# Performance work log

Measured on AMD Instinct MI355X. Metric: run time of the kernel, lower is better.

## Reference

```python
import jax, jax.numpy as jnp
import numpy as np

NUM_GROUPS = 4
EPS = 1e-6


def group_norm(x, scale, bias):
    # x: (b, c, f, h, w), normalize per group over (c//G, f, h, w) in fp32
    b, c, f, h, w = x.shape
    xg = x.astype(jnp.float32).reshape(b, NUM_GROUPS, c // NUM_GROUPS, f, h, w)
    mean = xg.mean(axis=(2, 3, 4, 5), keepdims=True)
    var = xg.var(axis=(2, 3, 4, 5), keepdims=True)
    xn = ((xg - mean) * jax.lax.rsqrt(var + EPS)).reshape(b, c, f, h, w)
    return (xn * scale[None, :, None, None, None] + bias[None, :, None, None, None]).astype(x.dtype)


def conv1x1x1(x, w, b):
    # 1x1x1 Conv3d == channel-mixing linear. w: (c_out, c_in), b: (c_out,)
    return jnp.einsum('bcfhw,oc->bofhw', x, w) + b[None, :, None, None, None]


def setup_inputs() -> dict:
    key = jax.random.key(0)
    ks = jax.random.split(key, 9)
    c = 256
    x = jax.random.normal(ks[0], (6, c, 48, 48), dtype=jnp.float32)  # (3*b, c, h, w), b=2
    init = lambda k: (jax.random.normal(k, (c, c), dtype=jnp.float32) * 0.02)
    return {
        'x': x,
        'gn_scale': jnp.ones((c,), jnp.float32),
        'gn_bias': jnp.zeros((c,), jnp.float32),
        'wq': init(ks[1]), 'bq': jnp.zeros((c,), jnp.float32),
        'wk': init(ks[2]), 'bk': jnp.zeros((c,), jnp.float32),
        'wv': init(ks[3]), 'bv': jnp.zeros((c,), jnp.float32),
        'wp': init(ks[4]), 'bp': jnp.zeros((c,), jnp.float32),
    }


def reference(x, gn_scale, gn_bias, wq, bq, wk, bk, wv, bv, wp, bp):
    b3, c, hh, ww = x.shape
    b = b3 // 3
    # chunk(x, 3) along batch, stack at dim 2 -> (b, c, f=3, h, w)
    h_ = x.reshape(3, b, c, hh, ww).transpose(1, 2, 0, 3, 4)
    h_ = group_norm(h_, gn_scale, gn_bias)
    q = conv1x1x1(h_, wq, bq)
    k = conv1x1x1(h_, wk, bk)
    v = conv1x1x1(h_, wv, bv)
    f = 3
    n = f * hh * ww
    qf = q.reshape(b, c, n).transpose(0, 2, 1)  # (b, n, c)
    kf = k.reshape(b, c, n)                     # (b, c, n)
    vf = v.reshape(b, c, n)                     # (b, c, n)
    scale = jnp.float32(c) ** -0.5
    scores = jnp.einsum('bic,bcj->bij', qf.astype(jnp.float32), kf.astype(jnp.float32)) * scale
    attn = jax.nn.softmax(scores, axis=2).astype(x.dtype)  # (b, n, n)
    # bmm(v, attn^T): out[b,c,i] = sum_j v[b,c,j] * attn[b,i,j]
    h_ = jnp.einsum('bcj,bij->bci', vf, attn).reshape(b, c, f, hh, ww)
    h_ = conv1x1x1(h_, wp, bp)
    # (b, c, f, h, w) -> (b, f, c, h, w) -> (b*f, c, h, w)
    h_ = h_.transpose(0, 2, 1, 3, 4).reshape(b * f, c, hh, ww)
    return x + h_
```

## Files before the change

kernel.cpp:

```cpp
#include <hip/hip_runtime.h>
#include <hip/hip_bf16.h>

#define NPOS 6912
#define HW   2304
#define C    256
#define EPSG 1e-6f
#define K2 (0.0625f * 1.4426950408889634f)

typedef __attribute__((ext_vector_type(8))) short bf16x8;
typedef __attribute__((ext_vector_type(4))) float f32x4;
typedef __attribute__((ext_vector_type(16))) float f32x16;
typedef __attribute__((ext_vector_type(8))) int v8i;
typedef long long i64;
typedef unsigned char u8;

__device__ __forceinline__ unsigned short f2bf(float f) {
    union { float f; unsigned int u; } v; v.f = f;
    unsigned int lsb = (v.u >> 16) & 1u;
    return (unsigned short)((v.u + 0x7fffu + lsb) >> 16);
}

__device__ __forceinline__ u8 f2fp8(float f) {
    union { float f; unsigned u; } v; v.f = f;
    unsigned sgn = (v.u >> 24) & 0x80u;
    unsigned a = v.u & 0x7FFFFFFFu;
    if (a >= 0x3C800000u) {
        unsigned r = a + 0x000FFFFFu + ((a >> 20) & 1u);
        return (u8)(sgn | ((r >> 20) - 0x3C0u));
    }
    union { unsigned u; float f; } w2; w2.u = a;
    int mnt = (int)rintf(w2.f * 512.0f);
    return (u8)(sgn | (unsigned)mnt);
}

__device__ __forceinline__ float fp8tof(u8 v) {
    unsigned u = ((unsigned)(v & 0x80u) << 24) | ((((unsigned)(v & 0x7Fu)) + 960u) << 20);
    union { unsigned u; float f; } w; w.u = u;
    return w.f;
}

#define MFMA(a, b, c)  __builtin_amdgcn_mfma_f32_16x16x32_bf16((a), (b), (c), 0, 0, 0)
#define MFMAS16(a, b, c) __builtin_amdgcn_mfma_scale_f32_16x16x128_f8f6f4((a), (b), (c), 0, 0, 0, 0x7F7F7F7F, 0, 0x7F7F7F7F)
#define MFMAS32(a, b, c) __builtin_amdgcn_mfma_scale_f32_32x32x64_f8f6f4((a), (b), (c), 0, 0, 0, 0x7F7F7F7F, 0, 0x7F7F7F7F)

__device__ __forceinline__ v8i mk8(int4 lo, int4 hi) {
    v8i r;
    r[0] = lo.x; r[1] = lo.y; r[2] = lo.z; r[3] = lo.w;
    r[4] = hi.x; r[5] = hi.y; r[6] = hi.z; r[7] = hi.w;
    return r;
}

__device__ __forceinline__ void gld16(const u8* g, const char* l) {
    __builtin_amdgcn_global_load_lds(
        (const __attribute__((address_space(1))) void*)(unsigned long long)g,
        (__attribute__((address_space(3))) void*)(unsigned int)(unsigned long long)l,
        16, 0, 0);
}


__global__ __launch_bounds__(256) void gn_stats(const float* x, float* part,
                                                const float* wq, const float* wk,
                                                const float* wv, const float* wp,
                                                unsigned short* wbf) {
    if (blockIdx.x < 256) {
        int i = blockIdx.x * 256 + threadIdx.x;
        int o = i >> 8, c = i & 255;
        int pos = (((o >> 6) * 4 + ((o >> 4) & 3)) * 8 + (c >> 5)) * 512
                + (((c >> 3) & 3) * 16 + (o & 15)) * 8 + (c & 7);
        wbf[pos]          = f2bf(wq[i]);
        wbf[65536 + pos]  = f2bf(wk[i]);
        wbf[131072 + pos] = f2bf(wv[i]);
        wbf[196608 + pos] = f2bf(wp[i]);
    }
    int gid = blockIdx.x / 108, slice = blockIdx.x % 108;
    int b = gid >> 2, grp = gid & 3;
    float s = 0.f, s2 = 0.f;
    #pragma unroll
    for (int k = 0; k < 16; ++k) {
        int e = slice * 4096 + k * 256 + (int)threadIdx.x;
        int f = e / 147456; int r1 = e - f * 147456;
        int ch = r1 / HW;   int sp = r1 - ch * HW;
        float v = x[(size_t)((f * 2 + b) * C + grp * 64 + ch) * HW + sp];
        s += v; s2 += v * v;
    }
    #pragma unroll
    for (int off = 32; off; off >>= 1) { s += __shfl_xor(s, off); s2 += __shfl_xor(s2, off); }
    __shared__ float ls[8];
    int w = threadIdx.x >> 6;
    if ((threadIdx.x & 63) == 0) { ls[w * 2] = s; ls[w * 2 + 1] = s2; }
    __syncthreads();
    if (threadIdx.x == 0) {
        float t = 0.f, t2 = 0.f;
        for (int i2 = 0; i2 < 4; ++i2) { t += ls[i2 * 2]; t2 += ls[i2 * 2 + 1]; }
        part[blockIdx.x * 2] = t; part[blockIdx.x * 2 + 1] = t2;
    }
}

__global__ __launch_bounds__(256) void gn_apply(const float* x, const float* part,
                                                const float* gsc, const float* gbi,
                                                unsigned short* hnf) {
    int blk = blockIdx.x;
    int b = blk / 144; int f = (blk % 144) / 48; int y = blk % 48;
    int c = threadIdx.x;
    int gid = b * 4 + (c >> 6);
    float s = 0.f, s2 = 0.f;
    for (int i = 0; i < 108; ++i) {
        s  += part[(gid * 108 + i) * 2];
        s2 += part[(gid * 108 + i) * 2 + 1];
    }
    float mean = s / 442368.f;
    float rsig = rsqrtf(s2 / 442368.f - mean * mean + EPSG);
    float sc = gsc[c] * rsig, bi = gbi[c] - mean * sc;
    __shared__ unsigned short lds[48 * 256];
    const float* xr = x + (size_t)((f * 2 + b) * C + c) * HW + y * 48;
    #pragma unroll
    for (int xw = 0; xw < 48; xw += 4) {
        float4 v = *(const float4*)(xr + xw);
        lds[(xw + 0) * 256 + c] = f2bf(v.x * sc + bi);
        lds[(xw + 1) * 256 + c] = f2bf(v.y * sc + bi);
        lds[(xw + 2) * 256 + c] = f2bf(v.z * sc + bi);
        lds[(xw + 3) * 256 + c] = f2bf(v.w * sc + bi);
    }
    __syncthreads();
    int kc = c >> 5, gg = (c >> 3) & 3, j = c & 7;
    int nbase = f * HW + y * 48;
    for (int xw = 0; xw < 48; ++xw) {
        int n = nbase + xw;
        size_t idx = ((size_t)(((b * 108 + (n >> 6)) * 4 + ((n >> 4) & 3)) * 8 + kc)) * 512
                   + (gg * 16 + (n & 15)) * 8 + j;
        hnf[idx] = lds[xw * 256 + c];
    }
}

__global__ __launch_bounds__(256) void qkv_gemm(const unsigned short* hnf, const unsigned short* wbf,
                                                const float* bq, const float* bk, const float* bvp,
                                                u8* qfp, u8* kfp, u8* vfp) {
    __shared__ u8 tr[4096];
    int t = blockIdx.x;
    int tid = (int)threadIdx.x;
    int lane = tid & 63, w = tid >> 6;
    int l16 = lane & 15, g = lane >> 4;
    f32x4 acc[4] = {{0.f,0.f,0.f,0.f},{0.f,0.f,0.f,0.f},{0.f,0.f,0.f,0.f},{0.f,0.f,0.f,0.f}};
    if (t < 1728) {
        int sel = t / 864; int rem = t % 864;
        int b = rem / 432;  int rem2 = rem % 432;
        int pt = rem2 >> 2; int ot = rem2 & 3;
        const unsigned short* wsel = wbf + sel * 65536;
        const float* bias = sel ? bk : bq;
        u8* out = sel ? kfp : qfp;
        const unsigned short* af  = hnf + (size_t)(((b * 108 + pt) * 4 + w) * 8) * 512 + lane * 8;
        const unsigned short* bfm = wsel + (size_t)(ot * 4 * 8) * 512 + lane * 8;
        #pragma unroll
        for (int kk = 0; kk < 8; ++kk) {
            bf16x8 a = *(const bf16x8*)(af + kk * 512);
            #pragma unroll
            for (int f = 0; f < 4; ++f) {
                bf16x8 bb = *(const bf16x8*)(bfm + (f * 8 + kk) * 512);
                acc[f] = MFMA(a, bb, acc[f]);
            }
        }
        #pragma unroll
        for (int f = 0; f < 4; ++f) {
            float bv = bias[ot * 64 + f * 16 + l16];
            #pragma unroll
            for (int r = 0; r < 4; ++r)
                tr[w * 1024 + (f & 1) * 512 + ((f >> 1) * 16 + 4 * g + r) * 16 + l16]
                    = f2fp8(acc[f][r] + bv);
        }
        __syncthreads();
        int t2 = tid >> 6, hf = (tid >> 5) & 1, ln = tid & 31;
        size_t frag = ((size_t)(b * 108 + pt) * 4 + t2) * 2 + (ot >> 1);
        *(int4*)(out + frag * 2048 + hf * 1024 + ((ot & 1) * 32 + ln) * 16)
            = *(const int4*)(tr + tid * 16);
    } else {
        int tv = t - 1728;
        int b = tv / 432; int rem2 = tv % 432;
        int ot = rem2 / 108; int pt = rem2 % 108;
        const unsigned short* wvw = wbf + 131072;
        const unsigned short* afm = wvw + (size_t)((ot * 4 + w) * 8) * 512 + lane * 8;
        const unsigned short* bfm = hnf + (size_t)((b * 108 + pt) * 4 * 8) * 512 + lane * 8;
        #pragma unroll
        for (int kk = 0; kk < 8; ++kk) {
            bf16x8 a = *(const bf16x8*)(afm + kk * 512);
            #pragma unroll
            for (int f = 0; f < 4; ++f) {
                bf16x8 bb = *(const bf16x8*)(bfm + (f * 8 + kk) * 512);
                acc[f] = MFMA(a, bb, acc[f]);
            }
        }
        #pragma unroll
        for (int f = 0; f < 4; ++f) {
            #pragma unroll
            for (int r = 0; r < 4; ++r) {
                int o = ot * 64 + w * 16 + 4 * g + r;
                tr[(w >> 1) * 2048 + (f & 1) * 1024
                   + ((f >> 1) * 32 + (w & 1) * 16 + 4 * g + r) * 16 + l16]
                    = f2fp8(acc[f][r] + bvp[o]);
            }
        }
        __syncthreads();
        size_t frag = (size_t)(b * 108 + pt) * 8 + ot * 2 + (tid >> 7);
        *(int4*)(vfp + frag * 2048 + (tid & 127) * 16) = *(const int4*)(tr + tid * 16);
    }
}

__global__ __launch_bounds__(512, 2) void flash(const u8* qf, const u8* kf, const u8* vf,
                                                u8* po, float* lsg) {
    __shared__ char smem[81920];
    int blk = blockIdx.x;
    int x = blk & 7, qt = blk >> 3;
    int b = x >> 2, ks = x & 3;
    int slot = ks * 2 + b;
    int tid = (int)threadIdx.x;
    int lane = tid & 63, w = tid >> 6;
    int l16 = lane & 15, g = lane >> 4;
    int i0 = qt * 256 + w * 32;

    v8i qa[2][2];
    #pragma unroll
    for (int u = 0; u < 2; ++u)
        #pragma unroll
        for (int h = 0; h < 2; ++h) {
            const u8* qb = qf + ((((size_t)b * 108 + qt * 4 + (w >> 1)) * 4
                                  + ((2 * w + u) & 3)) * 2 + h) * 2048 + lane * 16;
            qa[u][h] = mk8(*(const int4*)qb, *(const int4*)(qb + 1024));
        }

    size_t tb = (size_t)(b * 108 + ks * 27) * 16384;
    const u8* kst[2]; const u8* vst[2];
    #pragma unroll
    for (int q = 0; q < 2; ++q) {
        kst[q] = kf + tb + (q * 8 + w) * 1024 + lane * 16;
        vst[q] = vf + tb + (q * 8 + w) * 1024 + lane * 16;
    }
    #pragma unroll
    for (int q = 0; q < 2; ++q) {
        gld16(kst[q], smem + (q * 8 + w) * 1024);
        gld16(vst[q], smem + 16384 + (q * 8 + w) * 1024);
        kst[q] += 16384; vst[q] += 16384;
    }

    f32x16 oacc[8];
    #pragma unroll
    for (int ct = 0; ct < 8; ++ct)
        #pragma unroll
        for (int r = 0; r < 16; ++r) oacc[ct][r] = 0.f;
    float lsum0 = 0.f, lsum1 = 0.f;
    int pbase = 65536 + w * 2048;

    __syncthreads();

    for (int it = 0; it < 27; ++it) {
        int cur = it & 1;
        if (it < 26) {
            int db = (cur ^ 1) * 32768;
            #pragma unroll
            for (int q = 0; q < 2; ++q) {
                gld16(kst[q], smem + db + (q * 8 + w) * 1024);
                gld16(vst[q], smem + db + 16384 + (q * 8 + w) * 1024);
                kst[q] += 16384; vst[q] += 16384;
            }
        }
        int kb = cur * 32768;
        int vb = kb + 16384;

        f32x4 s4[2][4];
        #pragma unroll
        for (int u = 0; u < 2; ++u)
            #pragma unroll
            for (int tt = 0; tt < 4; ++tt) s4[u][tt] = (f32x4){0.f,0.f,0.f,0.f};
        __builtin_amdgcn_s_setprio(1);
        #pragma unroll
        for (int tt = 0; tt < 4; ++tt) {
            #pragma unroll
            for (int h = 0; h < 2; ++h) {
                const char* ka = smem + kb + (tt * 2 + h) * 2048 + lane * 16;
                v8i a = mk8(*(const int4*)ka, *(const int4*)(ka + 1024));
                s4[0][tt] = MFMAS16(a, qa[0][h], s4[0][tt]);
                s4[1][tt] = MFMAS16(a, qa[1][h], s4[1][tt]);
            }
        }
        __builtin_amdgcn_s_setprio(0);

        #pragma unroll
        for (int u = 0; u < 2; ++u) {
            float rs = 0.f;
            #pragma unroll
            for (int tt = 0; tt < 4; ++tt) {
                float p0 = __builtin_amdgcn_exp2f(fminf(s4[u][tt][0] * K2, 8.f));
                float p1 = __builtin_amdgcn_exp2f(fminf(s4[u][tt][1] * K2, 8.f));
                float p2 = __builtin_amdgcn_exp2f(fminf(s4[u][tt][2] * K2, 8.f));
                float p3 = __builtin_amdgcn_exp2f(fminf(s4[u][tt][3] * K2, 8.f));
                rs += (p0 + p1) + (p2 + p3);
                int lo = __builtin_amdgcn_cvt_pk_fp8_f32(p0, p1, 0, false);
                int d  = __builtin_amdgcn_cvt_pk_fp8_f32(p2, p3, lo, true);
                *(int*)(smem + pbase + u * 1024 + (tt >> 1) * 512 + l16 * 32
                        + (tt & 1) * 16 + g * 4) = d;
            }
            rs += __shfl_xor(rs, 16);
            rs += __shfl_xor(rs, 32);
            if (u == 0) lsum0 += rs; else lsum1 += rs;
        }

        {
            const char* pp = smem + pbase + ((lane >> 4) & 1) * 1024 + (lane >> 5) * 512
                           + l16 * 32;
            v8i pa = mk8(*(const int4*)pp, *(const int4*)(pp + 16));
            __builtin_amdgcn_s_setprio(1);
            #pragma unroll
            for (int ct = 0; ct < 8; ++ct) {
                const char* va = smem + vb + ct * 2048 + lane * 16;
                v8i vv = mk8(*(const int4*)va, *(const int4*)(va + 1024));
                oacc[ct] = MFMAS32(pa, vv, oacc[ct]);
            }
            __builtin_amdgcn_s_setprio(0);
        }
        __syncthreads();
    }

    #pragma unroll
    for (int ct = 0; ct < 8; ++ct)
        #pragma unroll
        for (int r = 0; r < 16; ++r) {
            int n = i0 + (r & 3) + 8 * (r >> 2) + 4 * (lane >> 5);
            po[((size_t)slot * NPOS + n) * C + ct * 32 + (lane & 31)] = f2fp8(oacc[ct][r]);
        }
    if (lane < 16) {
        lsg[(size_t)slot * NPOS + i0 + lane]      = lsum0;
        lsg[(size_t)slot * NPOS + i0 + 16 + lane] = lsum1;
    }
}

__global__ __launch_bounds__(256) void proj(const u8* po, const float* lsg,
                                            const unsigned short* wbf,
                                            const float* bp, const float* x, float* out) {
    int t = blockIdx.x;
    int b = t / 432; int rem2 = t % 432;
    int pt = rem2 >> 2; int ot = rem2 & 3;
    int lane = threadIdx.x & 63, w = threadIdx.x >> 6;
    int l16 = lane & 15, g = lane >> 4;
    int n = pt * 64 + w * 16 + l16;
    float l = 0.f;
    #pragma unroll
    for (int ks2 = 0; ks2 < 4; ++ks2) l += lsg[(size_t)(ks2 * 2 + b) * NPOS + n];
    float rl = 1.f / l;
    const unsigned short* wpw = wbf + 196608;
    const unsigned short* bfm = wpw + (size_t)(ot * 4 * 8) * 512 + lane * 8;
    const u8* prow = po + ((size_t)b * NPOS + n) * C + g * 8;
    f32x4 acc[4] = {{0.f,0.f,0.f,0.f},{0.f,0.f,0.f,0.f},{0.f,0.f,0.f,0.f},{0.f,0.f,0.f,0.f}};
    #pragma unroll
    for (int kk = 0; kk < 8; ++kk) {
        float av0 = 0.f, av1 = 0.f, av2 = 0.f, av3 = 0.f;
        float av4 = 0.f, av5 = 0.f, av6 = 0.f, av7 = 0.f;
        #pragma unroll
        for (int ks2 = 0; ks2 < 4; ++ks2) {
            i64 p8 = *(const i64*)(prow + (size_t)ks2 * (2 * NPOS * 256) + kk * 32);
            av0 += fp8tof((u8)(p8));        av1 += fp8tof((u8)(p8 >> 8));
            av2 += fp8tof((u8)(p8 >> 16));  av3 += fp8tof((u8)(p8 >> 24));
            av4 += fp8tof((u8)(p8 >> 32));  av5 += fp8tof((u8)(p8 >> 40));
            av6 += fp8tof((u8)(p8 >> 48));  av7 += fp8tof((u8)(p8 >> 56));
        }
        bf16x8 a;
        a[0] = (short)f2bf(av0 * rl); a[1] = (short)f2bf(av1 * rl);
        a[2] = (short)f2bf(av2 * rl); a[3] = (short)f2bf(av3 * rl);
        a[4] = (short)f2bf(av4 * rl); a[5] = (short)f2bf(av5 * rl);
        a[6] = (short)f2bf(av6 * rl); a[7] = (short)f2bf(av7 * rl);
        #pragma unroll
        for (int f = 0; f < 4; ++f) {
            bf16x8 bb = *(const bf16x8*)(bfm + (f * 8 + kk) * 512);
            acc[f] = MFMA(a, bb, acc[f]);
        }
    }
    __shared__ float lt[64][72];
    #pragma unroll
    for (int f = 0; f < 4; ++f) {
        float bv = bp[ot * 64 + f * 16 + l16];
        #pragma unroll
        for (int r = 0; r < 4; ++r)
            lt[f * 16 + l16][w * 16 + 4 * g + r] = acc[f][r] + bv;
    }
    __syncthreads();
    int p0 = pt * 64;
    int f3 = p0 / HW; int sp0 = p0 - f3 * HW;
    for (int it = 0; it < 16; ++it) {
        int ol = it * 4 + w;
        int pl = lane;
        size_t idx = ((size_t)(b * 3 + f3) * C + ot * 64 + ol) * HW + sp0 + pl;
        out[idx] = x[idx] + lt[ol][pl];
    }
}

extern "C" void kernel_launch(void* const* d_in, const int* in_sizes, int n_in,
                              void* d_out, int out_size, void* d_ws, size_t ws_size,
                              hipStream_t stream) {
    const float* x   = (const float*)d_in[0];
    const float* gsc = (const float*)d_in[1];
    const float* gbi = (const float*)d_in[2];
    const float* wq  = (const float*)d_in[3];
    const float* bq  = (const float*)d_in[4];
    const float* wk  = (const float*)d_in[5];
    const float* bk  = (const float*)d_in[6];
    const float* wv  = (const float*)d_in[7];
    const float* bv  = (const float*)d_in[8];
    const float* wp  = (const float*)d_in[9];
    const float* bp  = (const float*)d_in[10];

    char* ws = (char*)d_ws;
    unsigned short* wbf = (unsigned short*)(ws);
    float* part         = (float*)(ws + 524288);
    unsigned short* hn  = (unsigned short*)(ws + 532480);
    u8* qfp             = (u8*)(ws + 7610368);
    u8* kfp             = (u8*)(ws + 11149312);
    u8* vfp             = (u8*)(ws + 14688256);
    u8* po              = (u8*)(ws + 18227200);
    float* lsg          = (float*)(ws + 32382976);
    float* out = (float*)d_out;

    hipLaunchKernelGGL(gn_stats, dim3(864),  dim3(256), 0, stream, x, part, wq, wk, wv, wp, wbf);
    hipLaunchKernelGGL(gn_apply, dim3(288),  dim3(256), 0, stream, x, part, gsc, gbi, hn);
    hipLaunchKernelGGL(qkv_gemm, dim3(2592), dim3(256), 0, stream, hn, wbf, bq, bk, bv, qfp, kfp, vfp);
    hipLaunchKernelGGL(flash,    dim3(216),  dim3(512), 0, stream, qfp, kfp, vfp, po, lsg);
    hipLaunchKernelGGL(proj,     dim3(864),  dim3(256), 0, stream, po, lsg, wbf, bp, x, out);
}
```

Measured before the change: 141.6 us.

## Triple-buffer K/V tiles and software-pipeline QK^T one step ahead of softmax-PV

Grows the LDS buffers in the flash kernel from two K/V stages to three, so loads are issued two iterations ahead. The loop is restructured so each step computes the next tile's QK^T scores into a second register set while running exp/convert and the PV MFMAs for the current tile, using ping-pong score registers. The goal is to hide global-load latency and let MFMA work overlap the exp/convert VALU work. In exchange, LDS use rises to 112 KB per block, which may prevent two 512-thread blocks from fitting per CU, and the extra score registers raise register pressure.

```diff
diff --git a/kernel.cpp b/kernel.cpp
--- a/kernel.cpp
+++ b/kernel.cpp
@@ -206,7 +206,7 @@
 
 __global__ __launch_bounds__(512, 2) void flash(const u8* qf, const u8* kf, const u8* vf,
                                                 u8* po, float* lsg) {
-    __shared__ char smem[81920];
+    __shared__ char smem[114688];
     int blk = blockIdx.x;
     int x = blk & 7, qt = blk >> 3;
     int b = x >> 2, ks = x & 3;
@@ -239,6 +239,12 @@
         gld16(vst[q], smem + 16384 + (q * 8 + w) * 1024);
         kst[q] += 16384; vst[q] += 16384;
     }
+    #pragma unroll
+    for (int q = 0; q < 2; ++q) {
+        gld16(kst[q], smem + 32768 + (q * 8 + w) * 1024);
+        gld16(vst[q], smem + 32768 + 16384 + (q * 8 + w) * 1024);
+        kst[q] += 16384; vst[q] += 16384;
+    }
 
     f32x16 oacc[8];
     #pragma unroll
@@ -246,77 +252,100 @@
         #pragma unroll
         for (int r = 0; r < 16; ++r) oacc[ct][r] = 0.f;
     float lsum0 = 0.f, lsum1 = 0.f;
-    int pbase = 65536 + w * 2048;
+    int pbase = 98304 + w * 2048;
+    f32x4 sA[2][4], sB[2][4];
+    int bc = 0, bn = 32768, bs = 65536;
 
     __syncthreads();
 
-    for (int it = 0; it < 27; ++it) {
-        int cur = it & 1;
-        if (it < 26) {
-            int db = (cur ^ 1) * 32768;
-            #pragma unroll
-            for (int q = 0; q < 2; ++q) {
-                gld16(kst[q], smem + db + (q * 8 + w) * 1024);
-                gld16(vst[q], smem + db + 16384 + (q * 8 + w) * 1024);
-                kst[q] += 16384; vst[q] += 16384;
+    {
+        #pragma unroll
+        for (int u = 0; u < 2; ++u)
+            #pragma unroll
+            for (int tt = 0; tt < 4; ++tt) sA[u][tt] = (f32x4){0.f,0.f,0.f,0.f};
+        __builtin_amdgcn_s_setprio(1);
+        #pragma unroll
+        for (int tt = 0; tt < 4; ++tt)
+            #pragma unroll
+            for (int h = 0; h < 2; ++h) {
+                const char* ka = smem + (tt * 2 + h) * 2048 + lane * 16;
+                v8i a = mk8(*(const int4*)ka, *(const int4*)(ka + 1024));
+                sA[0][tt] = MFMAS16(a, qa[0][h], sA[0][tt]);
+                sA[1][tt] = MFMAS16(a, qa[1][h], sA[1][tt]);
             }
-        }
-        int kb = cur * 32768;
-        int vb = kb + 16384;
-
-        f32x4 s4[2][4];
-        #pragma unroll
-        for (int u = 0; u < 2; ++u)
-            #pragma unroll
-            for (int tt = 0; tt < 4; ++tt) s4[u][tt] = (f32x4){0.f,0.f,0.f,0.f};
-        __builtin_amdgcn_s_setprio(1);
-        #pragma unroll
-        for (int tt = 0; tt < 4; ++tt) {
-            #pragma unroll
-            for (int h = 0; h < 2; ++h) {
-                const char* ka = smem + kb + (tt * 2 + h) * 2048 + lane * 16;
-                v8i a = mk8(*(const int4*)ka, *(const int4*)(ka + 1024));
-                s4[0][tt] = MFMAS16(a, qa[0][h], s4[0][tt]);
-                s4[1][tt] = MFMAS16(a, qa[1][h], s4[1][tt]);
-            }
-        }
         __builtin_amdgcn_s_setprio(0);
-
-        #pragma unroll
-        for (int u = 0; u < 2; ++u) {
-            float rs = 0.f;
-            #pragma unroll
-            for (int tt = 0; tt < 4; ++tt) {
-                float p0 = __builtin_amdgcn_exp2f(fminf(s4[u][tt][0] * K2, 8.f));
-                float p1 = __builtin_amdgcn_exp2f(fminf(s4[u][tt][1] * K2, 8.f));
-                float p2 = __builtin_amdgcn_exp2f(fminf(s4[u][tt][2] * K2, 8.f));
-                float p3 = __builtin_amdgcn_exp2f(fminf(s4[u][tt][3] * K2, 8.f));
-                rs += (p0 + p1) + (p2 + p3);
-                int lo = __builtin_amdgcn_cvt_pk_fp8_f32(p0, p1, 0, false);
-                int d  = __builtin_amdgcn_cvt_pk_fp8_f32(p2, p3, lo, true);
-                *(int*)(smem + pbase + u * 1024 + (tt >> 1) * 512 + l16 * 32
-                        + (tt & 1) * 16 + g * 4) = d;
-            }
-            rs += __shfl_xor(rs, 16);
-            rs += __shfl_xor(rs, 32);
-            if (u == 0) lsum0 += rs; else lsum1 += rs;
-        }
-
-        {
-            const char* pp = smem + pbase + ((lane >> 4) & 1) * 1024 + (lane >> 5) * 512
-                           + l16 * 32;
-            v8i pa = mk8(*(const int4*)pp, *(const int4*)(pp + 16));
-            __builtin_amdgcn_s_setprio(1);
-            #pragma unroll
-            for (int ct = 0; ct < 8; ++ct) {
-                const char* va = smem + vb + ct * 2048 + lane * 16;
-                v8i vv = mk8(*(const int4*)va, *(const int4*)(va + 1024));
-                oacc[ct] = MFMAS32(pa, vv, oacc[ct]);
-            }
-            __builtin_amdgcn_s_setprio(0);
-        }
-        __syncthreads();
-    }
+    }
+
+#define FBODY(T, SCUR, SNXT) {                                                    \
+    __syncthreads();                                                              \
+    if ((T) + 2 < 27) {                                                           \
+        _Pragma("unroll")                                                         \
+        for (int q = 0; q < 2; ++q) {                                             \
+            gld16(kst[q], smem + bs + (q * 8 + w) * 1024);                        \
+            gld16(vst[q], smem + bs + 16384 + (q * 8 + w) * 1024);                \
+            kst[q] += 16384; vst[q] += 16384;                                     \
+        }                                                                         \
+    }                                                                             \
+    if ((T) + 1 < 27) {                                                           \
+        _Pragma("unroll")                                                         \
+        for (int u = 0; u < 2; ++u) {                                             \
+            _Pragma("unroll")                                                     \
+            for (int tt = 0; tt < 4; ++tt) SNXT[u][tt] = (f32x4){0.f,0.f,0.f,0.f};\
+        }                                                                         \
+        __builtin_amdgcn_s_setprio(1);                                            \
+        _Pragma("unroll")                                                         \
+        for (int tt = 0; tt < 4; ++tt) {                                          \
+            _Pragma("unroll")                                                     \
+            for (int h = 0; h < 2; ++h) {                                         \
+                const char* ka = smem + bn + (tt * 2 + h) * 2048 + lane * 16;     \
+                v8i a = mk8(*(const int4*)ka, *(const int4*)(ka + 1024));         \
+                SNXT[0][tt] = MFMAS16(a, qa[0][h], SNXT[0][tt]);                  \
+                SNXT[1][tt] = MFMAS16(a, qa[1][h], SNXT[1][tt]);                  \
+            }                                                                     \
+        }                                                                         \
+        __builtin_amdgcn_s_setprio(0);                                            \
+    }                                                                             \
+    _Pragma("unroll")                                                             \
+    for (int u = 0; u < 2; ++u) {                                                 \
+        float rs = 0.f;                                                           \
+        _Pragma("unroll")                                                         \
+        for (int tt = 0; tt < 4; ++tt) {                                          \
+            float p0 = __builtin_amdgcn_exp2f(fminf(SCUR[u][tt][0] * K2, 8.f));   \
+            float p1 = __builtin_amdgcn_exp2f(fminf(SCUR[u][tt][1] * K2, 8.f));   \
+            float p2 = __builtin_amdgcn_exp2f(fminf(SCUR[u][tt][2] * K2, 8.f));   \
+            float p3 = __builtin_amdgcn_exp2f(fminf(SCUR[u][tt][3] * K2, 8.f));   \
+            rs += (p0 + p1) + (p2 + p3);                                          \
+            int lo = __builtin_amdgcn_cvt_pk_fp8_f32(p0, p1, 0, false);           \
+            int d  = __builtin_amdgcn_cvt_pk_fp8_f32(p2, p3, lo, true);           \
+            *(int*)(smem + pbase + u * 1024 + (tt >> 1) * 512 + l16 * 32          \
+                    + (tt & 1) * 16 + g * 4) = d;                                 \
+        }                                                                         \
+        rs += __shfl_xor(rs, 16);                                                 \
+        rs += __shfl_xor(rs, 32);                                                 \
+        if (u == 0) lsum0 += rs; else lsum1 += rs;                                \
+    }                                                                             \
+    {                                                                             \
+        const char* pp = smem + pbase + ((lane >> 4) & 1) * 1024                  \
+                       + (lane >> 5) * 512 + l16 * 32;                            \
+        v8i pa = mk8(*(const int4*)pp, *(const int4*)(pp + 16));                  \
+        __builtin_amdgcn_s_setprio(1);                                            \
+        _Pragma("unroll")                                                         \
+        for (int ct = 0; ct < 8; ++ct) {                                          \
+            const char* va = smem + bc + 16384 + ct * 2048 + lane * 16;           \
+            v8i vv = mk8(*(const int4*)va, *(const int4*)(va + 1024));            \
+            oacc[ct] = MFMAS32(pa, vv, oacc[ct]);                                 \
+        }                                                                         \
+        __builtin_amdgcn_s_setprio(0);                                            \
+    }                                                                             \
+    { int _t = bc; bc = bn; bn = bs; bs = _t; }                                   \
+}
+
+    for (int t = 0; t < 26; t += 2) {
+        FBODY(t, sA, sB);
+        FBODY(t + 1, sB, sA);
+    }
+    FBODY(26, sA, sB);
+#undef FBODY
 
     #pragma unroll
     for (int ct = 0; ct < 8; ++ct)
```

Result: slower. 371.4 us (+162.2%).

## Triple-buffer K/V tiles and software-pipeline QK^T ahead of PV in flash kernel

Applied to the files above, without the earlier changes.

Moves K/V staging in LDS from double to triple buffering, prefetching two tiles ahead with rotating buffer offsets. Each step now computes the QK^T scores for the next tile before the PV MFMAs of the current tile, so score MFMAs can overlap the softmax/P-write latency. The loop keeps a single barrier per step, now at the top. The cost is LDS per block rising from 80 KB to 112 KB, which probably stops two 512-thread blocks from sharing a CU. It also adds live score registers across the loop.

```diff
diff --git a/kernel.cpp b/kernel.cpp
--- a/kernel.cpp
+++ b/kernel.cpp
@@ -206,7 +206,7 @@
 
 __global__ __launch_bounds__(512, 2) void flash(const u8* qf, const u8* kf, const u8* vf,
                                                 u8* po, float* lsg) {
-    __shared__ char smem[81920];
+    __shared__ char smem[114688];
     int blk = blockIdx.x;
     int x = blk & 7, qt = blk >> 3;
     int b = x >> 2, ks = x & 3;
@@ -239,6 +239,12 @@
         gld16(vst[q], smem + 16384 + (q * 8 + w) * 1024);
         kst[q] += 16384; vst[q] += 16384;
     }
+    #pragma unroll
+    for (int q = 0; q < 2; ++q) {
+        gld16(kst[q], smem + 32768 + (q * 8 + w) * 1024);
+        gld16(vst[q], smem + 32768 + 16384 + (q * 8 + w) * 1024);
+        kst[q] += 16384; vst[q] += 16384;
+    }
 
     f32x16 oacc[8];
     #pragma unroll
@@ -246,41 +252,38 @@
         #pragma unroll
         for (int r = 0; r < 16; ++r) oacc[ct][r] = 0.f;
     float lsum0 = 0.f, lsum1 = 0.f;
-    int pbase = 65536 + w * 2048;
+    int pbase = 98304 + w * 2048;
+    f32x4 s4[2][4];
+    int bc = 0, bn = 32768, bs = 65536;
 
     __syncthreads();
 
-    for (int it = 0; it < 27; ++it) {
-        int cur = it & 1;
-        if (it < 26) {
-            int db = (cur ^ 1) * 32768;
+    #pragma unroll
+    for (int u = 0; u < 2; ++u)
+        #pragma unroll
+        for (int tt = 0; tt < 4; ++tt) s4[u][tt] = (f32x4){0.f,0.f,0.f,0.f};
+    __builtin_amdgcn_s_setprio(1);
+    #pragma unroll
+    for (int tt = 0; tt < 4; ++tt)
+        #pragma unroll
+        for (int h = 0; h < 2; ++h) {
+            const char* ka = smem + (tt * 2 + h) * 2048 + lane * 16;
+            v8i a = mk8(*(const int4*)ka, *(const int4*)(ka + 1024));
+            s4[0][tt] = MFMAS16(a, qa[0][h], s4[0][tt]);
+            s4[1][tt] = MFMAS16(a, qa[1][h], s4[1][tt]);
+        }
+    __builtin_amdgcn_s_setprio(0);
+
+    for (int t = 0; t < 27; ++t) {
+        __syncthreads();
+        if (t + 2 < 27) {
             #pragma unroll
             for (int q = 0; q < 2; ++q) {
-                gld16(kst[q], smem + db + (q * 8 + w) * 1024);
-                gld16(vst[q], smem + db + 16384 + (q * 8 + w) * 1024);
+                gld16(kst[q], smem + bs + (q * 8 + w) * 1024);
+                gld16(vst[q], smem + bs + 16384 + (q * 8 + w) * 1024);
                 kst[q] += 16384; vst[q] += 16384;
             }
         }
-        int kb = cur * 32768;
-        int vb = kb + 16384;
-
-        f32x4 s4[2][4];
-        #pragma unroll
-        for (int u = 0; u < 2; ++u)
-            #pragma unroll
-            for (int tt = 0; tt < 4; ++tt) s4[u][tt] = (f32x4){0.f,0.f,0.f,0.f};
-        __builtin_amdgcn_s_setprio(1);
-        #pragma unroll
-        for (int tt = 0; tt < 4; ++tt) {
-            #pragma unroll
-            for (int h = 0; h < 2; ++h) {
-                const char* ka = smem + kb + (tt * 2 + h) * 2048 + lane * 16;
-                v8i a = mk8(*(const int4*)ka, *(const int4*)(ka + 1024));
-                s4[0][tt] = MFMAS16(a, qa[0][h], s4[0][tt]);
-                s4[1][tt] = MFMAS16(a, qa[1][h], s4[1][tt]);
-            }
-        }
-        __builtin_amdgcn_s_setprio(0);
 
         #pragma unroll
         for (int u = 0; u < 2; ++u) {
@@ -302,6 +305,24 @@
             if (u == 0) lsum0 += rs; else lsum1 += rs;
         }
 
+        if (t + 1 < 27) {
+            #pragma unroll
+            for (int u = 0; u < 2; ++u)
+                #pragma unroll
+                for (int tt = 0; tt < 4; ++tt) s4[u][tt] = (f32x4){0.f,0.f,0.f,0.f};
+            __builtin_amdgcn_s_setprio(1);
+            #pragma unroll
+            for (int tt = 0; tt < 4; ++tt)
+                #pragma unroll
+                for (int h = 0; h < 2; ++h) {
+                    const char* ka = smem + bn + (tt * 2 + h) * 2048 + lane * 16;
+                    v8i a = mk8(*(const int4*)ka, *(const int4*)(ka + 1024));
+                    s4[0][tt] = MFMAS16(a, qa[0][h], s4[0][tt]);
+                    s4[1][tt] = MFMAS16(a, qa[1][h], s4[1][tt]);
+                }
+            __builtin_amdgcn_s_setprio(0);
+        }
+
         {
             const char* pp = smem + pbase + ((lane >> 4) & 1) * 1024 + (lane >> 5) * 512
                            + l16 * 32;
@@ -309,13 +330,13 @@
             __builtin_amdgcn_s_setprio(1);
             #pragma unroll
             for (int ct = 0; ct < 8; ++ct) {
-                const char* va = smem + vb + ct * 2048 + lane * 16;
+                const char* va = smem + bc + 16384 + ct * 2048 + lane * 16;
                 v8i vv = mk8(*(const int4*)va, *(const int4*)(va + 1024));
                 oacc[ct] = MFMAS32(pa, vv, oacc[ct]);
             }
             __builtin_amdgcn_s_setprio(0);
         }
-        __syncthreads();
+        int tmp = bc; bc = bn; bn = bs; bs = tmp;
     }
 
     #pragma unroll
```

Result: faster. 135.7 us (median of 2 runs) (-4.2%).
